# Optimization experiments

Hardware: AMD Instinct MI355X
Metric: run time of the kernel (lower is better)

The kernel has to match this reference:

```python
import jax, jax.numpy as jnp
import numpy as np

NUM_HEADS = 2
LN_EPS = 1e-5


def setup_inputs() -> dict:
    key = jax.random.key(0)
    ks = jax.random.split(key, 4)
    bs, C, H, W = 32, 512, 64, 64
    T, token_dim = 64, 128
    features = jax.random.normal(ks[0], (bs, C, H, W), dtype=jnp.float32)
    tokens = jax.random.normal(ks[1], (T, bs, token_dim), dtype=jnp.float32)
    q_w = jax.random.normal(ks[2], (C, token_dim), dtype=jnp.float32) * (token_dim ** -0.5)
    q_b = jnp.zeros((C,), dtype=jnp.float32)
    proj_w = jax.random.normal(ks[3], (token_dim, C), dtype=jnp.float32) * (C ** -0.5)
    proj_b = jnp.zeros((token_dim,), dtype=jnp.float32)
    ln_w = jnp.ones((token_dim,), dtype=jnp.float32)
    ln_b = jnp.zeros((token_dim,), dtype=jnp.float32)
    return {"features": features, "tokens": tokens, "q_w": q_w, "q_b": q_b,
            "proj_w": proj_w, "proj_b": proj_b, "ln_w": ln_w, "ln_b": ln_b}


def reference(features, tokens, q_w, q_b, proj_w, proj_b, ln_w, ln_b):
    bs, C, H, W = features.shape
    T = tokens.shape[0]
    nh = NUM_HEADS
    ch = C // nh
    scale = ch ** -0.5
    # q projection: [T, bs, token_dim] -> [T, bs, C] -> [bs, nh, T, ch]
    t = (tokens @ q_w.T + q_b).reshape(T, bs, nh, ch).transpose(1, 2, 0, 3)
    # keys (reused as values): [bs, nh, ch, H*W]
    k = features.reshape(bs, nh, ch, H * W)
    # attention scores over spatial positions
    attn = jnp.einsum('bhtc,bhcs->bhts', t, k) * scale  # [bs, nh, T, HW]
    a = jax.nn.softmax(attn, axis=-1)
    attn_out = jnp.einsum('bhts,bhcs->bhtc', a, k)      # [bs, nh, T, ch]
    # back to [T, bs, C], project, residual, layernorm
    t_a = attn_out.transpose(2, 0, 1, 3).reshape(T, bs, C)
    t_a = t_a @ proj_w.T + proj_b
    tok = tokens + t_a
    mu = jnp.mean(tok, axis=-1, keepdims=True)
    var = jnp.var(tok, axis=-1, keepdims=True)
    tok = (tok - mu) * jax.lax.rsqrt(var + LN_EPS) * ln_w + ln_b
    return tok, attn.reshape(bs, nh, T, H, W)
```

## Files before the change

### kernel.cpp

```cpp
#include <hip/hip_runtime.h>
#include <stdint.h>
#include <stddef.h>

typedef __attribute__((ext_vector_type(8))) __bf16 bf16x8;
typedef __attribute__((ext_vector_type(4))) float f32x4;

#define NC 8
#define SCHUNK 512
#define SS 32
#define NSUB 16
#define KTP 256
#define PP 40

#define MFMA __builtin_amdgcn_mfma_f32_16x16x32_bf16

__global__ __launch_bounds__(128) void k_qproj(
    const float* __restrict__ tokens, const float* __restrict__ q_w,
    const float* __restrict__ q_b, __bf16* __restrict__ ws_q)
{
    const int t = blockIdx.x >> 3;
    const int b0 = (blockIdx.x & 7) * 4;
    const int d = threadIdx.x;
    __shared__ float tok[4][128];
    #pragma unroll
    for (int j = 0; j < 4; ++j)
        tok[j][d] = tokens[((size_t)t * 32 + b0 + j) * 128 + d];
    __syncthreads();
    #pragma unroll
    for (int i = 0; i < 4; ++i) {
        const int c = d + 128 * i;
        const float* wr = q_w + (size_t)c * 128;
        const float qb = q_b[c];
        float acc[4] = {qb, qb, qb, qb};
        #pragma unroll 4
        for (int k = 0; k < 128; k += 4) {
            const float4 w4 = *(const float4*)(wr + k);
            #pragma unroll
            for (int j = 0; j < 4; ++j) {
                const float4 t4 = *(const float4*)&tok[j][k];
                acc[j] += t4.x * w4.x + t4.y * w4.y + t4.z * w4.z + t4.w * w4.w;
            }
        }
        const int h = c >> 8, cc = c & 255;
        #pragma unroll
        for (int j = 0; j < 4; ++j)
            ws_q[(size_t)(((b0 + j) * 2 + h) * 64 + t) * 256 + cc] = (__bf16)acc[j];
    }
}

__global__ __launch_bounds__(256, 2) void k_attn(
    const float* __restrict__ feat, const __bf16* __restrict__ ws_q,
    float* __restrict__ attn_g, float* __restrict__ part, float* __restrict__ zbuf)
{
    const int bh = blockIdx.x >> 3;
    const int nc = blockIdx.x & 7;
    const int b = bh >> 1, h = bh & 1;
    const int tid = threadIdx.x;
    const int lane = tid & 63;
    const int w = tid >> 6;
    const int l15 = lane & 15, g = lane >> 4;
    const int t0 = w * 16;

    __shared__ __bf16 kT[SS * KTP];
    __shared__ __bf16 P[64 * PP];

    bf16x8 afr[8];
    {
        const __bf16* qb = ws_q + ((size_t)bh * 64 + t0 + l15) * 256 + g * 8;
        #pragma unroll
        for (int kk = 0; kk < 8; ++kk)
            afr[kk] = *(const bf16x8*)(qb + kk * 32);
    }

    f32x4 acc[16];
    #pragma unroll
    for (int i = 0; i < 16; ++i) { acc[i][0]=0.f; acc[i][1]=0.f; acc[i][2]=0.f; acc[i][3]=0.f; }
    float zp[4] = {0.f, 0.f, 0.f, 0.f};

    const float* fsrc = feat + ((size_t)b * 512 + (size_t)h * 256) * 4096
                      + (size_t)(w * 64 + l15) * 4096 + nc * SCHUNK + g * 8;

    float4 f4[8];
    #pragma unroll
    for (int ct = 0; ct < 4; ++ct) {
        f4[2*ct]   = *(const float4*)(fsrc + (size_t)ct * 16 * 4096);
        f4[2*ct+1] = *(const float4*)(fsrc + (size_t)ct * 16 * 4096 + 4);
    }

    bf16x8 kreg[4];

    #pragma unroll 1
    for (int ss = 0; ss < NSUB; ++ss) {
        __syncthreads();
        if (ss > 0) {
            #pragma unroll
            for (int tt = 0; tt < 4; ++tt) {
                const bf16x8 pa = *(const bf16x8*)&P[(tt * 16 + l15) * PP + g * 8];
                #pragma unroll
                for (int ct = 0; ct < 4; ++ct)
                    acc[tt * 4 + ct] = MFMA(pa, kreg[ct], acc[tt * 4 + ct], 0, 0, 0);
            }
        }
        #pragma unroll
        for (int ct = 0; ct < 4; ++ct) {
            const float4 a = f4[2*ct], c4 = f4[2*ct+1];
            bf16x8 kv;
            kv[0]=(__bf16)a.x;  kv[1]=(__bf16)a.y;  kv[2]=(__bf16)a.z;  kv[3]=(__bf16)a.w;
            kv[4]=(__bf16)c4.x; kv[5]=(__bf16)c4.y; kv[6]=(__bf16)c4.z; kv[7]=(__bf16)c4.w;
            kreg[ct] = kv;
            const int c = w * 64 + ct * 16 + l15;
            #pragma unroll
            for (int j = 0; j < 8; ++j) {
                const int s = g * 8 + j;
                kT[s * KTP + (c ^ ((s & 15) << 3))] = kv[j];
            }
        }
        if (ss < NSUB - 1) {
            const float* p2 = fsrc + (ss + 1) * SS;
            #pragma unroll
            for (int ct = 0; ct < 4; ++ct) {
                f4[2*ct]   = *(const float4*)(p2 + (size_t)ct * 16 * 4096);
                f4[2*ct+1] = *(const float4*)(p2 + (size_t)ct * 16 * 4096 + 4);
            }
        }
        __syncthreads();
        const int sw = nc * SCHUNK + ss * SS;
        #pragma unroll
        for (int nt = 0; nt < 2; ++nt) {
            f32x4 d; d[0]=0.f; d[1]=0.f; d[2]=0.f; d[3]=0.f;
            #pragma unroll
            for (int kk = 0; kk < 8; ++kk) {
                const int cc = kk * 32 + g * 8;
                const bf16x8 bfr = *(const bf16x8*)&kT[(nt * 16 + l15) * KTP + (cc ^ (l15 << 3))];
                d = MFMA(afr[kk], bfr, d, 0, 0, 0);
            }
            #pragma unroll
            for (int r = 0; r < 4; ++r) {
                const int t = t0 + g * 4 + r;
                const float sv = d[r] * 0.0625f;
                attn_g[((size_t)bh * 64 + t) * 4096 + sw + nt * 16 + l15] = sv;
                const float p = __expf(sv);
                zp[r] += p;
                P[t * PP + nt * 16 + l15] = (__bf16)p;
            }
        }
    }
    __syncthreads();
    #pragma unroll
    for (int tt = 0; tt < 4; ++tt) {
        const bf16x8 pa = *(const bf16x8*)&P[(tt * 16 + l15) * PP + g * 8];
        #pragma unroll
        for (int ct = 0; ct < 4; ++ct)
            acc[tt * 4 + ct] = MFMA(pa, kreg[ct], acc[tt * 4 + ct], 0, 0, 0);
    }

    const size_t pbase = (size_t)(bh * NC + nc) * 64 * 256;
    #pragma unroll
    for (int tt = 0; tt < 4; ++tt)
        #pragma unroll
        for (int ct = 0; ct < 4; ++ct)
            #pragma unroll
            for (int r = 0; r < 4; ++r)
                part[pbase + (size_t)(tt * 16 + g * 4 + r) * 256 + w * 64 + ct * 16 + l15]
                    = acc[tt * 4 + ct][r];
    #pragma unroll
    for (int r = 0; r < 4; ++r) {
        float z = zp[r];
        z += __shfl_xor(z, 1); z += __shfl_xor(z, 2);
        z += __shfl_xor(z, 4); z += __shfl_xor(z, 8);
        if (l15 == 0) zbuf[(size_t)(bh * NC + nc) * 64 + t0 + g * 4 + r] = z;
    }
}

__global__ __launch_bounds__(128) void k_post(
    const float* __restrict__ tokens, const float* __restrict__ proj_w,
    const float* __restrict__ proj_b, const float* __restrict__ ln_w,
    const float* __restrict__ ln_b, const float* __restrict__ part,
    const float* __restrict__ zbuf, float* __restrict__ out_tok)
{
    const int t = blockIdx.x >> 3;
    const int b0 = (blockIdx.x & 7) * 4;
    const int d = threadIdx.x;
    __shared__ float av[4][512];
    __shared__ float Zs[4][2];
    __shared__ float red[2][4][2];

    #pragma unroll
    for (int bb = 0; bb < 4; ++bb) {
        const int b = b0 + bb;
        #pragma unroll
        for (int i = 0; i < 4; ++i) {
            const int c = d + 128 * i;
            const int bh = b * 2 + (c >> 8), cc = c & 255;
            float s = 0.f;
            #pragma unroll
            for (int nc = 0; nc < NC; ++nc)
                s += part[((size_t)(bh * NC + nc) * 64 + t) * 256 + cc];
            av[bb][c] = s;
        }
    }
    if (d < 8) {
        const int bb = d >> 1, hh = d & 1;
        const int bh = (b0 + bb) * 2 + hh;
        float z = 0.f;
        for (int nc = 0; nc < NC; ++nc) z += zbuf[(size_t)(bh * NC + nc) * 64 + t];
        Zs[bb][hh] = z;
    }
    __syncthreads();
    #pragma unroll
    for (int bb = 0; bb < 4; ++bb) {
        const float rz0 = 1.f / Zs[bb][0], rz1 = 1.f / Zs[bb][1];
        #pragma unroll
        for (int i = 0; i < 4; ++i) {
            const int c = d + 128 * i;
            av[bb][c] *= (c < 256) ? rz0 : rz1;
        }
    }
    __syncthreads();

    const float pb = proj_b[d];
    float acc4[4] = {pb, pb, pb, pb};
    const float* wr = proj_w + (size_t)d * 512;
    #pragma unroll 4
    for (int k = 0; k < 512; k += 4) {
        const float4 w4 = *(const float4*)(wr + k);
        #pragma unroll
        for (int bb = 0; bb < 4; ++bb) {
            const float4 a4 = *(const float4*)&av[bb][k];
            acc4[bb] += a4.x * w4.x + a4.y * w4.y + a4.z * w4.z + a4.w * w4.w;
        }
    }
    float r[4], s1[4], s2[4];
    #pragma unroll
    for (int bb = 0; bb < 4; ++bb) {
        r[bb] = tokens[((size_t)t * 32 + b0 + bb) * 128 + d] + acc4[bb];
        s1[bb] = r[bb]; s2[bb] = r[bb] * r[bb];
    }
    #pragma unroll
    for (int o = 1; o < 64; o <<= 1)
        #pragma unroll
        for (int bb = 0; bb < 4; ++bb) {
            s1[bb] += __shfl_xor(s1[bb], o);
            s2[bb] += __shfl_xor(s2[bb], o);
        }
    const int wv = d >> 6;
    if ((d & 63) == 0)
        #pragma unroll
        for (int bb = 0; bb < 4; ++bb) { red[0][bb][wv] = s1[bb]; red[1][bb][wv] = s2[bb]; }
    __syncthreads();
    #pragma unroll
    for (int bb = 0; bb < 4; ++bb) {
        const float mean = (red[0][bb][0] + red[0][bb][1]) * (1.f / 128.f);
        const float ex2  = (red[1][bb][0] + red[1][bb][1]) * (1.f / 128.f);
        const float var = ex2 - mean * mean;
        out_tok[((size_t)t * 32 + b0 + bb) * 128 + d] =
            (r[bb] - mean) * rsqrtf(var + 1e-5f) * ln_w[d] + ln_b[d];
    }
}

extern "C" void kernel_launch(void* const* d_in, const int* in_sizes, int n_in,
                              void* d_out, int out_size, void* d_ws, size_t ws_size,
                              hipStream_t stream) {
    const float* features = (const float*)d_in[0];
    const float* tokens   = (const float*)d_in[1];
    const float* q_w      = (const float*)d_in[2];
    const float* q_b      = (const float*)d_in[3];
    const float* proj_w   = (const float*)d_in[4];
    const float* proj_b   = (const float*)d_in[5];
    const float* ln_w     = (const float*)d_in[6];
    const float* ln_b     = (const float*)d_in[7];

    float* out = (float*)d_out;
    float* out_attn = out + (size_t)64 * 32 * 128;

    __bf16* ws_q = (__bf16*)d_ws;
    float* part = (float*)((char*)d_ws + (size_t)2 * 1024 * 1024);
    float* zbuf = part + (size_t)64 * NC * 64 * 256;

    k_qproj<<<512, 128, 0, stream>>>(tokens, q_w, q_b, ws_q);
    k_attn<<<64 * NC, 256, 0, stream>>>(features, ws_q, out_attn, part, zbuf);
    k_post<<<512, 128, 0, stream>>>(tokens, proj_w, proj_b, ln_w, ln_b, part, zbuf, out);
}
```

Measured before the change: 138.2 us.

## Double attention sub-tile width and store partial outputs in bf16

Measured after the change: 224.9 us. 62.7% more time.

```diff
diff --git a/kernel.cpp b/kernel.cpp
--- a/kernel.cpp
+++ b/kernel.cpp
@@ -7,10 +7,10 @@
 
 #define NC 8
 #define SCHUNK 512
-#define SS 32
-#define NSUB 16
+#define SS 64
+#define NSUB 8
 #define KTP 256
-#define PP 40
+#define PP 72
 
 #define MFMA __builtin_amdgcn_mfma_f32_16x16x32_bf16
 
@@ -50,7 +50,7 @@
 
 __global__ __launch_bounds__(256, 2) void k_attn(
     const float* __restrict__ feat, const __bf16* __restrict__ ws_q,
-    float* __restrict__ attn_g, float* __restrict__ part, float* __restrict__ zbuf)
+    float* __restrict__ attn_g, __bf16* __restrict__ part, float* __restrict__ zbuf)
 {
     const int bh = blockIdx.x >> 3;
     const int nc = blockIdx.x & 7;
@@ -80,53 +80,61 @@
     const float* fsrc = feat + ((size_t)b * 512 + (size_t)h * 256) * 4096
                       + (size_t)(w * 64 + l15) * 4096 + nc * SCHUNK + g * 8;
 
-    float4 f4[8];
-    #pragma unroll
-    for (int ct = 0; ct < 4; ++ct) {
-        f4[2*ct]   = *(const float4*)(fsrc + (size_t)ct * 16 * 4096);
-        f4[2*ct+1] = *(const float4*)(fsrc + (size_t)ct * 16 * 4096 + 4);
-    }
-
-    bf16x8 kreg[4];
+    float4 f4[16];
+    #pragma unroll
+    for (int ct = 0; ct < 4; ++ct)
+        #pragma unroll
+        for (int ks = 0; ks < 2; ++ks) {
+            f4[ct*4 + ks*2 + 0] = *(const float4*)(fsrc + (size_t)ct * 16 * 4096 + ks * 32);
+            f4[ct*4 + ks*2 + 1] = *(const float4*)(fsrc + (size_t)ct * 16 * 4096 + ks * 32 + 4);
+        }
+
+    bf16x8 kreg[8];
 
     #pragma unroll 1
     for (int ss = 0; ss < NSUB; ++ss) {
         __syncthreads();
         if (ss > 0) {
             #pragma unroll
-            for (int tt = 0; tt < 4; ++tt) {
-                const bf16x8 pa = *(const bf16x8*)&P[(tt * 16 + l15) * PP + g * 8];
+            for (int tt = 0; tt < 4; ++tt)
                 #pragma unroll
-                for (int ct = 0; ct < 4; ++ct)
-                    acc[tt * 4 + ct] = MFMA(pa, kreg[ct], acc[tt * 4 + ct], 0, 0, 0);
-            }
-        }
-        #pragma unroll
-        for (int ct = 0; ct < 4; ++ct) {
-            const float4 a = f4[2*ct], c4 = f4[2*ct+1];
-            bf16x8 kv;
-            kv[0]=(__bf16)a.x;  kv[1]=(__bf16)a.y;  kv[2]=(__bf16)a.z;  kv[3]=(__bf16)a.w;
-            kv[4]=(__bf16)c4.x; kv[5]=(__bf16)c4.y; kv[6]=(__bf16)c4.z; kv[7]=(__bf16)c4.w;
-            kreg[ct] = kv;
-            const int c = w * 64 + ct * 16 + l15;
-            #pragma unroll
-            for (int j = 0; j < 8; ++j) {
-                const int s = g * 8 + j;
-                kT[s * KTP + (c ^ ((s & 15) << 3))] = kv[j];
-            }
-        }
+                for (int ks = 0; ks < 2; ++ks) {
+                    const bf16x8 pa = *(const bf16x8*)&P[(tt * 16 + l15) * PP + ks * 32 + g * 8];
+                    #pragma unroll
+                    for (int ct = 0; ct < 4; ++ct)
+                        acc[tt * 4 + ct] = MFMA(pa, kreg[ct*2 + ks], acc[tt * 4 + ct], 0, 0, 0);
+                }
+        }
+        #pragma unroll
+        for (int ct = 0; ct < 4; ++ct)
+            #pragma unroll
+            for (int ks = 0; ks < 2; ++ks) {
+                const float4 a = f4[ct*4 + ks*2], c4 = f4[ct*4 + ks*2 + 1];
+                bf16x8 kv;
+                kv[0]=(__bf16)a.x;  kv[1]=(__bf16)a.y;  kv[2]=(__bf16)a.z;  kv[3]=(__bf16)a.w;
+                kv[4]=(__bf16)c4.x; kv[5]=(__bf16)c4.y; kv[6]=(__bf16)c4.z; kv[7]=(__bf16)c4.w;
+                kreg[ct*2 + ks] = kv;
+                const int c = w * 64 + ct * 16 + l15;
+                #pragma unroll
+                for (int j = 0; j < 8; ++j) {
+                    const int s = ks * 32 + g * 8 + j;
+                    kT[s * KTP + (c ^ ((s & 15) << 3))] = kv[j];
+                }
+            }
+        __syncthreads();
         if (ss < NSUB - 1) {
             const float* p2 = fsrc + (ss + 1) * SS;
             #pragma unroll
-            for (int ct = 0; ct < 4; ++ct) {
-                f4[2*ct]   = *(const float4*)(p2 + (size_t)ct * 16 * 4096);
-                f4[2*ct+1] = *(const float4*)(p2 + (size_t)ct * 16 * 4096 + 4);
-            }
-        }
-        __syncthreads();
+            for (int ct = 0; ct < 4; ++ct)
+                #pragma unroll
+                for (int ks = 0; ks < 2; ++ks) {
+                    f4[ct*4 + ks*2 + 0] = *(const float4*)(p2 + (size_t)ct * 16 * 4096 + ks * 32);
+                    f4[ct*4 + ks*2 + 1] = *(const float4*)(p2 + (size_t)ct * 16 * 4096 + ks * 32 + 4);
+                }
+        }
         const int sw = nc * SCHUNK + ss * SS;
         #pragma unroll
-        for (int nt = 0; nt < 2; ++nt) {
+        for (int nt = 0; nt < 4; ++nt) {
             f32x4 d; d[0]=0.f; d[1]=0.f; d[2]=0.f; d[3]=0.f;
             #pragma unroll
             for (int kk = 0; kk < 8; ++kk) {
@@ -147,12 +155,14 @@
     }
     __syncthreads();
     #pragma unroll
-    for (int tt = 0; tt < 4; ++tt) {
-        const bf16x8 pa = *(const bf16x8*)&P[(tt * 16 + l15) * PP + g * 8];
-        #pragma unroll
-        for (int ct = 0; ct < 4; ++ct)
-            acc[tt * 4 + ct] = MFMA(pa, kreg[ct], acc[tt * 4 + ct], 0, 0, 0);
-    }
+    for (int tt = 0; tt < 4; ++tt)
+        #pragma unroll
+        for (int ks = 0; ks < 2; ++ks) {
+            const bf16x8 pa = *(const bf16x8*)&P[(tt * 16 + l15) * PP + ks * 32 + g * 8];
+            #pragma unroll
+            for (int ct = 0; ct < 4; ++ct)
+                acc[tt * 4 + ct] = MFMA(pa, kreg[ct*2 + ks], acc[tt * 4 + ct], 0, 0, 0);
+        }
 
     const size_t pbase = (size_t)(bh * NC + nc) * 64 * 256;
     #pragma unroll
@@ -162,7 +172,7 @@
             #pragma unroll
             for (int r = 0; r < 4; ++r)
                 part[pbase + (size_t)(tt * 16 + g * 4 + r) * 256 + w * 64 + ct * 16 + l15]
-                    = acc[tt * 4 + ct][r];
+                    = (__bf16)acc[tt * 4 + ct][r];
     #pragma unroll
     for (int r = 0; r < 4; ++r) {
         float z = zp[r];
@@ -175,7 +185,7 @@
 __global__ __launch_bounds__(128) void k_post(
     const float* __restrict__ tokens, const float* __restrict__ proj_w,
     const float* __restrict__ proj_b, const float* __restrict__ ln_w,
-    const float* __restrict__ ln_b, const float* __restrict__ part,
+    const float* __restrict__ ln_b, const __bf16* __restrict__ part,
     const float* __restrict__ zbuf, float* __restrict__ out_tok)
 {
     const int t = blockIdx.x >> 3;
@@ -195,7 +205,7 @@
             float s = 0.f;
             #pragma unroll
             for (int nc = 0; nc < NC; ++nc)
-                s += part[((size_t)(bh * NC + nc) * 64 + t) * 256 + cc];
+                s += (float)part[((size_t)(bh * NC + nc) * 64 + t) * 256 + cc];
             av[bb][c] = s;
         }
     }
@@ -274,8 +284,8 @@
     float* out_attn = out + (size_t)64 * 32 * 128;
 
     __bf16* ws_q = (__bf16*)d_ws;
-    float* part = (float*)((char*)d_ws + (size_t)2 * 1024 * 1024);
-    float* zbuf = part + (size_t)64 * NC * 64 * 256;
+    __bf16* part = (__bf16*)((char*)d_ws + (size_t)2 * 1024 * 1024);
+    float* zbuf = (float*)((char*)d_ws + (size_t)20 * 1024 * 1024);
 
     k_qproj<<<512, 128, 0, stream>>>(tokens, q_w, q_b, ws_q);
     k_attn<<<64 * NC, 256, 0, stream>>>(features, ws_q, out_attn, part, zbuf);
```
